# Kernel tuning notes

Measured on AMD Instinct MI355X. Metric: run time of the kernel, lower is better.

The kernel has to match this reference:

```python
import jax, jax.numpy as jnp
import numpy as np

HID, H, KV, D = 2048, 16, 4, 128
B, L = 8, 1024
T = B * L
EPS = 1e-6
NEG = -1e9


def _rms(x, w):
    # RMSNorm over head_dim in fp32
    var = jnp.mean(x.astype(jnp.float32) ** 2, axis=-1, keepdims=True)
    return (x.astype(jnp.float32) * jax.lax.rsqrt(var + EPS)).astype(x.dtype) * w


def _rot_half(x):
    x1, x2 = jnp.split(x, 2, axis=-1)
    return jnp.concatenate([-x2, x1], axis=-1)


def setup_inputs() -> dict:
    key = jax.random.key(0)
    ks = jax.random.split(key, 24)
    inp = {}
    inp['packed_sequence'] = jax.random.normal(ks[0], (T, HID), jnp.float32) * 0.02
    # RoPE tables: positions restart per sample
    pos = jnp.tile(jnp.arange(L, dtype=jnp.float32), B)  # [T]
    inv_freq = 1.0 / (10000.0 ** (jnp.arange(0, D, 2, dtype=jnp.float32) / D))
    ang = pos[:, None] * inv_freq[None, :]  # [T, D/2]
    inp['cos'] = jnp.concatenate([jnp.cos(ang), jnp.cos(ang)], axis=-1)
    inp['sin'] = jnp.concatenate([jnp.sin(ang), jnp.sin(ang)], axis=-1)
    # per-sample causal additive mask [B, L, L]
    causal = jnp.tril(jnp.ones((L, L), bool))
    inp['attn_bias'] = jnp.broadcast_to(jnp.where(causal, 0.0, NEG).astype(jnp.float32), (B, L, L))
    inp['gen_mask'] = jax.random.randint(ks[1], (T,), 0, 2, jnp.int32)
    s = 0.02
    inp['Wq'] = jax.random.normal(ks[2], (H * D, HID), jnp.float32) * s
    inp['bq'] = jnp.zeros((H * D,), jnp.float32)
    inp['Wqg'] = jax.random.normal(ks[3], (H * D, HID), jnp.float32) * s
    inp['bqg'] = jnp.zeros((H * D,), jnp.float32)
    inp['Wk'] = jax.random.normal(ks[4], (KV * D, HID), jnp.float32) * s
    inp['bk'] = jnp.zeros((KV * D,), jnp.float32)
    inp['Wkg'] = jax.random.normal(ks[5], (KV * D, HID), jnp.float32) * s
    inp['bkg'] = jnp.zeros((KV * D,), jnp.float32)
    inp['Wv'] = jax.random.normal(ks[6], (KV * D, HID), jnp.float32) * s
    inp['bv'] = jnp.zeros((KV * D,), jnp.float32)
    inp['Wvg'] = jax.random.normal(ks[7], (KV * D, HID), jnp.float32) * s
    inp['bvg'] = jnp.zeros((KV * D,), jnp.float32)
    inp['Wo'] = jax.random.normal(ks[8], (HID, H * D), jnp.float32) * s
    inp['Wog'] = jax.random.normal(ks[9], (HID, H * D), jnp.float32) * s
    inp['q_norm_w'] = jnp.ones((D,), jnp.float32)
    inp['q_norm_gen_w'] = jnp.ones((D,), jnp.float32)
    inp['k_norm_w'] = jnp.ones((D,), jnp.float32)
    inp['k_norm_gen_w'] = jnp.ones((D,), jnp.float32)
    return inp


def reference(packed_sequence, cos, sin, attn_bias, gen_mask,
              Wq, bq, Wqg, bqg, Wk, bk, Wkg, bkg, Wv, bv, Wvg, bvg,
              Wo, Wog, q_norm_w, q_norm_gen_w, k_norm_w, k_norm_gen_w):
    route = (gen_mask > 0)[:, None]  # [T,1]; und/gen indexes partition tokens -> select
    # dual-path QKV projections (scatter into zero buffers == per-token select)
    q = jnp.where(route, packed_sequence @ Wqg.T + bqg, packed_sequence @ Wq.T + bq)
    k = jnp.where(route, packed_sequence @ Wkg.T + bkg, packed_sequence @ Wk.T + bk)
    v = jnp.where(route, packed_sequence @ Wvg.T + bvg, packed_sequence @ Wv.T + bv)
    q = q.reshape(T, H, D)
    k = k.reshape(T, KV, D)
    v = v.reshape(T, KV, D)
    rh = route[:, :, None]  # [T,1,1]
    # dual-path per-head-dim RMSNorm
    q = jnp.where(rh, _rms(q, q_norm_gen_w), _rms(q, q_norm_w))
    k = jnp.where(rh, _rms(k, k_norm_gen_w), _rms(k, k_norm_w))
    # RoPE (broadcast over heads, unsqueeze_dim=1)
    c, s = cos[:, None, :], sin[:, None, :]
    q = q * c + _rot_half(q) * s
    k = k * c + _rot_half(k) * s
    # GQA: repeat kv heads to H
    k = jnp.repeat(k, H // KV, axis=1)
    v = jnp.repeat(v, H // KV, axis=1)
    # ragged attention, equal sample lens -> batched SDPA with per-sample masks
    qb = q.reshape(B, L, H, D)
    kb = k.reshape(B, L, H, D)
    vb = v.reshape(B, L, H, D)
    scores = jnp.einsum('blhd,bmhd->bhlm', qb, kb) / np.sqrt(D).astype(np.float32)
    scores = scores + attn_bias[:, None, :, :]
    p = jax.nn.softmax(scores, axis=-1)
    o = jnp.einsum('bhlm,bmhd->blhd', p, vb).reshape(T, H * D)
    # dual-path output projection (no bias)
    return jnp.where(route, o @ Wog.T, o @ Wo.T)
```

## Files before the change

kernel.cpp:

```cpp
#include <hip/hip_runtime.h>

#define T_TOK 8192
#define HID   2048
#define NH    16
#define NKV   4
#define HD    128

typedef __attribute__((ext_vector_type(8))) short short8;
typedef __attribute__((ext_vector_type(4))) float f32x4;
typedef __attribute__((ext_vector_type(4))) unsigned short us4;

__device__ __forceinline__ unsigned short f2b(float f) {
  union { float f; unsigned int u; } x; x.f = f;
  unsigned int u = x.u;
  return (unsigned short)((u + 0x7FFFu + ((u >> 16) & 1u)) >> 16);
}
__device__ __forceinline__ float b2f(unsigned short u) {
  union { float f; unsigned int u; } x; x.u = ((unsigned int)u) << 16; return x.f;
}

__device__ __forceinline__ void ld_lds16(const unsigned short* g, unsigned short* l) {
  __builtin_amdgcn_global_load_lds(
      (const __attribute__((address_space(1))) unsigned int*)g,
      (__attribute__((address_space(3))) unsigned int*)l, 16, 0, 0);
}

__device__ __forceinline__ int xcd_swz(int orig, int nwg) {
  int q = nwg >> 3;
  return (orig & 7) * q + (orig >> 3);
}

__device__ __forceinline__ void qkv_map(int orig, int& bx, int& by, int& set) {
  int xcd = orig & 7;
  int wl = orig >> 3;
  int g = wl / 96;
  int rem = wl - g * 96;
  int p = rem >> 1;
  int e = rem & 1;
  bx = (g * 2 + e) * 8 + xcd;
  set = p / 24; by = p - set * 24;
}
__device__ __forceinline__ void out_map(int orig, int& bx, int& by, int& set) {
  int xcd = orig & 7;
  int wl = orig >> 3;
  int g = wl / 64;
  int rem = wl - g * 64;
  int p = rem >> 1;
  int e = rem & 1;
  bx = (g * 2 + e) * 8 + xcd;
  set = p / 16; by = p - set * 16;
}

struct ConvArgs {
  const float* src[9];
  unsigned short* dst[9];
  int blk_end[9];
  const int* gm; int* perm; int* n0p;
};

__global__ __launch_bounds__(256) void convert_all(ConvArgs a) {
  int blk = blockIdx.x;
  int nconv = a.blk_end[8];
  if (blk == nconv) {
    __shared__ int cnt[256];
    int t = threadIdx.x;
    int base = t * 32;
    int c = 0;
#pragma unroll
    for (int i = 0; i < 32; i++) c += (a.gm[base + i] > 0) ? 0 : 1;
    cnt[t] = c;
    __syncthreads();
    for (int off = 1; off < 256; off <<= 1) {
      int add = (t >= off) ? cnt[t - off] : 0;
      __syncthreads();
      cnt[t] += add;
      __syncthreads();
    }
    int incl = cnt[t];
    int total0 = cnt[255];
    int p0 = incl - c;
    int p1 = total0 + base - p0;
#pragma unroll
    for (int i = 0; i < 32; i++) {
      int tok = base + i;
      if (a.gm[tok] > 0) a.perm[p1++] = tok;
      else               a.perm[p0++] = tok;
    }
    if (t == 0) a.n0p[0] = total0;
    return;
  }
  int s = 0;
  while (blk >= a.blk_end[s]) s++;
  int local = blk - (s ? a.blk_end[s - 1] : 0);
  int i = local * 1024 + threadIdx.x * 4;
  float4 v = *(const float4*)(a.src[s] + i);
  us4 o = { f2b(v.x), f2b(v.y), f2b(v.z), f2b(v.w) };
  *(us4*)(a.dst[s] + i) = o;
}

#define BM  128
#define BK  64

__device__ __forceinline__ void gemm_core(
    const unsigned short* __restrict__ Xb,
    const unsigned short* __restrict__ W,
    const float* __restrict__ bias,
    const int* __restrict__ perm,
    int r0, int r1, int col0, int N,
    float* __restrict__ outF, unsigned short* __restrict__ outB,
    unsigned short* As, unsigned short* Bs)
{
  int tid = threadIdx.x;
  int lane = tid & 63, wid = tid >> 6;
  int quad = lane >> 4, l15 = lane & 15;
  int wr = (wid >> 1) * 64, wc = (wid & 1) * 64;
  int lrow = lane >> 3;
  int sc8 = (lane & 7) ^ (lrow & 7);

  const unsigned short* ag[4]; const unsigned short* bg[4];
  unsigned short* al[4]; unsigned short* bl[4];
#pragma unroll
  for (int i = 0; i < 4; i++) {
    int row = wid * 32 + i * 8 + lrow;
    int gr = r0 + row; if (gr > r1 - 1) gr = r1 - 1;
    ag[i] = Xb + (size_t)perm[gr] * HID + sc8 * 8;
    bg[i] = W + (size_t)(col0 + row) * HID + sc8 * 8;
    al[i] = As + (wid * 32 + i * 8) * BK;
    bl[i] = Bs + (wid * 32 + i * 8) * BK;
  }

  f32x4 zero = {0.f, 0.f, 0.f, 0.f};
  f32x4 acc[4][4];
#pragma unroll
  for (int a = 0; a < 4; a++)
#pragma unroll
    for (int b = 0; b < 4; b++) acc[a][b] = zero;

  for (int k0 = 0; k0 < HID; k0 += BK) {
#pragma unroll
    for (int i = 0; i < 4; i++) {
      ld_lds16(ag[i] + k0, al[i]);
      ld_lds16(bg[i] + k0, bl[i]);
    }
    __syncthreads();
#pragma unroll
    for (int kk = 0; kk < 2; kk++) {
      int cswz = ((kk * 4 + quad) ^ (l15 & 7)) * 8;
      short8 af[4], bf[4];
#pragma unroll
      for (int mt = 0; mt < 4; mt++)
        af[mt] = *(const short8*)&As[(wr + mt * 16 + l15) * BK + cswz];
#pragma unroll
      for (int nt = 0; nt < 4; nt++)
        bf[nt] = *(const short8*)&Bs[(wc + nt * 16 + l15) * BK + cswz];
#pragma unroll
      for (int mt = 0; mt < 4; mt++)
#pragma unroll
        for (int nt = 0; nt < 4; nt++)
          acc[mt][nt] = __builtin_amdgcn_mfma_f32_16x16x32_bf16(af[mt], bf[nt], acc[mt][nt], 0, 0, 0);
    }
    __syncthreads();
  }

#pragma unroll
  for (int mt = 0; mt < 4; mt++) {
#pragma unroll
    for (int r = 0; r < 4; r++) {
      int lr = wr + mt * 16 + quad * 4 + r;
      int gr = r0 + lr;
      if (gr >= r1) continue;
      int tok = perm[gr];
#pragma unroll
      for (int nt = 0; nt < 4; nt++) {
        int col = col0 + wc + nt * 16 + l15;
        float v = acc[mt][nt][r];
        if (bias) v += bias[col];
        if (outF) outF[(size_t)tok * N + col] = v;
        else      outB[(size_t)tok * N + col] = f2b(v);
      }
    }
  }
}

#define QKV_GX 64
#define QKV_GY 24
__global__ __launch_bounds__(256, 3) void gemm_qkv(
    const unsigned short* __restrict__ xb,
    const unsigned short* wq0, const unsigned short* wq1,
    const float* bq0, const float* bq1,
    const unsigned short* wk0, const unsigned short* wk1,
    const float* bk0, const float* bk1,
    const unsigned short* wv0, const unsigned short* wv1,
    const float* bv0, const float* bv1,
    unsigned short* qraw, unsigned short* kraw, unsigned short* vb,
    const int* __restrict__ perm, const int* __restrict__ n0p)
{
  __shared__ unsigned short As[BM * BK];
  __shared__ unsigned short Bs[BM * BK];
  int orig = blockIdx.x + QKV_GX * (blockIdx.y + QKV_GY * blockIdx.z);
  int bx, by, set;
  qkv_map(orig, bx, by, set);

  int n0 = n0p[0];
  int r0, r1;
  if (set == 0) { r0 = bx * BM; if (r0 >= n0) return; r1 = (r0 + BM < n0) ? r0 + BM : n0; }
  else          { r0 = n0 + bx * BM; if (r0 >= T_TOK) return; r1 = (r0 + BM < T_TOK) ? r0 + BM : T_TOK; }
  const unsigned short* w; const float* bias;
  unsigned short* ob; int col0, N;
  if (by < 16)      { w = set ? wq1 : wq0; bias = set ? bq1 : bq0; col0 = by * 128;        N = HID; ob = qraw; }
  else if (by < 20) { w = set ? wk1 : wk0; bias = set ? bk1 : bk0; col0 = (by - 16) * 128; N = 512; ob = kraw; }
  else              { w = set ? wv1 : wv0; bias = set ? bv1 : bv0; col0 = (by - 20) * 128; N = 512; ob = vb; }
  gemm_core(xb, w, bias, perm, r0, r1, col0, N, nullptr, ob, As, Bs);
}

#define OUT_GX 64
#define OUT_GY 16
__global__ __launch_bounds__(256, 3) void gemm_out(
    const unsigned short* __restrict__ obuf,
    const unsigned short* wo0, const unsigned short* wo1,
    float* __restrict__ out,
    const int* __restrict__ perm, const int* __restrict__ n0p)
{
  __shared__ unsigned short As[BM * BK];
  __shared__ unsigned short Bs[BM * BK];
  int orig = blockIdx.x + OUT_GX * (blockIdx.y + OUT_GY * blockIdx.z);
  int bx, by, set;
  out_map(orig, bx, by, set);

  int n0 = n0p[0];
  int r0, r1;
  if (set == 0) { r0 = bx * BM; if (r0 >= n0) return; r1 = (r0 + BM < n0) ? r0 + BM : n0; }
  else          { r0 = n0 + bx * BM; if (r0 >= T_TOK) return; r1 = (r0 + BM < T_TOK) ? r0 + BM : T_TOK; }
  gemm_core(obuf, set ? wo1 : wo0, nullptr, perm, r0, r1, by * 128, HID, out, nullptr, As, Bs);
}

#define RR_BLOCKS (T_TOK * (NH + NKV) / 4)

__global__ __launch_bounds__(256) void rope_vtrans(
    const unsigned short* __restrict__ qin, unsigned short* __restrict__ qout,
    const unsigned short* __restrict__ kin, unsigned short* __restrict__ kout,
    const float* __restrict__ cosb, const float* __restrict__ sinb,
    const int* __restrict__ gm,
    const float* __restrict__ qwn, const float* __restrict__ qwg,
    const float* __restrict__ kwn, const float* __restrict__ kwg,
    const unsigned short* __restrict__ vb, unsigned short* __restrict__ vt)
{
  __shared__ unsigned short Vs[64][136];
  if (blockIdx.x >= RR_BLOCKS) {
    int idx = blockIdx.x - RR_BLOCKS;
    int kt = idx & 15, kvh = (idx >> 4) & 3, b = idx >> 6;
    int t = threadIdx.x;
    int kv0 = kt * 64;
    int key = t >> 2, c0 = t & 3;
#pragma unroll
    for (int i = 0; i < 4; i++) {
      int cc = c0 * 4 + i;
      *(short8*)&Vs[key][cc * 8] =
          *(const short8*)(vb + ((size_t)(b * 1024 + kv0 + key) * NKV + kvh) * HD + cc * 8);
    }
    __syncthreads();
    int d = t >> 1, hh = t & 1;
    unsigned short tmp[32];
#pragma unroll
    for (int k = 0; k < 32; k++) tmp[k] = Vs[hh * 32 + k][d];
    size_t base = ((size_t)(b * NKV + kvh) * HD + d) * 1024 + kv0 + hh * 32;
    *(short8*)(vt + base)      = *(short8*)&tmp[0];
    *(short8*)(vt + base + 8)  = *(short8*)&tmp[8];
    *(short8*)(vt + base + 16) = *(short8*)&tmp[16];
    *(short8*)(vt + base + 24) = *(short8*)&tmp[24];
    return;
  }
  int wvid = blockIdx.x * 4 + (threadIdx.x >> 6);
  int lane = threadIdx.x & 63;
  const unsigned short* in; unsigned short* outp;
  const float* wn; const float* wg; int t, h, nh;
  if (wvid < T_TOK * NH) {
    in = qin; outp = qout; wn = qwn; wg = qwg; t = wvid >> 4; h = wvid & 15; nh = NH;
  } else {
    int w2 = wvid - T_TOK * NH;
    in = kin; outp = kout; wn = kwn; wg = kwg; t = w2 >> 2; h = w2 & 3; nh = NKV;
  }
  size_t off = ((size_t)t * nh + h) * HD;
  float x1 = b2f(in[off + lane]), x2 = b2f(in[off + 64 + lane]);
  float ss = x1 * x1 + x2 * x2;
#pragma unroll
  for (int o = 32; o > 0; o >>= 1) ss += __shfl_xor(ss, o, 64);
  float inv = rsqrtf(ss * (1.0f / 128.0f) + 1e-6f);
  const float* w = (gm[t] > 0) ? wg : wn;
  float n1 = x1 * inv * w[lane];
  float n2 = x2 * inv * w[lane + 64];
  float c1 = cosb[t * HD + lane],      s1 = sinb[t * HD + lane];
  float c2 = cosb[t * HD + 64 + lane], s2 = sinb[t * HD + 64 + lane];
  outp[off + lane]      = f2b(n1 * c1 - n2 * s1);
  outp[off + 64 + lane] = f2b(n2 * c2 + n1 * s2);
}

__global__ __launch_bounds__(512, 4) void attn_kernel(
    const unsigned short* __restrict__ qb,
    const unsigned short* __restrict__ kb,
    const unsigned short* __restrict__ vt,
    unsigned short* __restrict__ ob)
{
  __shared__ unsigned short Ks[2][64 * 128];
  __shared__ unsigned short Vt[2][128 * 64];
  __shared__ unsigned short Ps[8 * 16 * 64];
  int orig = blockIdx.x + 16 * (blockIdx.y + 4 * blockIdx.z);
  int wg = xcd_swz(orig, 16 * 4 * 8);
  int pslot = wg % 16, kvh = (wg / 16) % 4, b = wg / 64;

  int tid = threadIdx.x, lane = tid & 63, wid = tid >> 6;
  int quad = lane >> 4, l15 = lane & 15;
  int h = kvh * 4 + (wid >> 1);
  int g = wid & 1;
  const float sc = 0.088388347648318447f;
  f32x4 zero = {0.f, 0.f, 0.f, 0.f};

  int skey = (wid << 2) + (lane >> 4);
  int kswz = ((lane & 15) ^ (skey & 7)) * 8;
  int sd   = (wid << 3) + (lane >> 3);
  int vswz = ((lane & 7) ^ (sd & 7)) * 8;

  auto stageKV = [&](int buf, int kv0) {
#pragma unroll
    for (int i = 0; i < 2; i++) {
      int key = i * 32 + skey;
      ld_lds16(kb + ((size_t)(b * 1024 + kv0 + key) * NKV + kvh) * HD + kswz,
               &Ks[buf][(size_t)(i * 32 + (wid << 2)) * 128]);
    }
#pragma unroll
    for (int i = 0; i < 2; i++) {
      int d = i * 64 + sd;
      ld_lds16(vt + ((size_t)(b * NKV + kvh) * HD + d) * 1024 + kv0 + vswz,
               &Vt[buf][(size_t)(i * 64 + (wid << 3)) * 64]);
    }
  };

  for (int half = 0; half < 2; half++) {
    int a = half ? (31 - pslot) : pslot;
    int q0 = a * 32;
    int qrow = q0 + g * 16 + l15;
    size_t qoff = ((size_t)(b * 1024 + qrow) * NH + h) * HD;
    short8 qfr[4];
#pragma unroll
    for (int kk = 0; kk < 4; kk++)
      qfr[kk] = *(const short8*)(qb + qoff + kk * 32 + quad * 8);

    f32x4 oacc[8];
#pragma unroll
    for (int i = 0; i < 8; i++) oacc[i] = zero;
    float lpart[4] = {0.f, 0.f, 0.f, 0.f};

    int ktiles = a / 2 + 1;
    stageKV(0, 0);
    int cur = 0;

    for (int kt = 0; kt < ktiles; kt++) {
      int kv0 = kt * 64;
      bool hasnext = (kt + 1 < ktiles);
      if (hasnext) {
        stageKV(cur ^ 1, kv0 + 64);
        asm volatile("s_waitcnt vmcnt(4)" ::: "memory");
      } else {
        asm volatile("s_waitcnt vmcnt(0)" ::: "memory");
      }
      __builtin_amdgcn_s_barrier();
      __builtin_amdgcn_sched_barrier(0);
      const unsigned short* ksb = Ks[cur];
      const unsigned short* vvb = Vt[cur];
      bool lastt = (kt == ktiles - 1);

      f32x4 s[4];
      __builtin_amdgcn_s_setprio(1);
#pragma unroll
      for (int g4 = 0; g4 < 4; g4++) {
        f32x4 acc = zero;
#pragma unroll
        for (int kk = 0; kk < 4; kk++) {
          short8 bfr = *(const short8*)&ksb[(g4 * 16 + l15) * 128 + ((kk * 4 + quad) ^ (l15 & 7)) * 8];
          acc = __builtin_amdgcn_mfma_f32_16x16x32_bf16(qfr[kk], bfr, acc, 0, 0, 0);
        }
        s[g4] = acc;
      }
      __builtin_amdgcn_s_setprio(0);

      int rowb = q0 + g * 16 + quad * 4;
#pragma unroll
      for (int g4 = 0; g4 < 4; g4++) {
        int col = kv0 + g4 * 16 + l15;
        int k8 = g4 * 2 + (l15 >> 3);
#pragma unroll
        for (int r = 0; r < 4; r++) {
          float p = __expf(s[g4][r] * sc);
          if (lastt && col > rowb + r) p = 0.f;
          lpart[r] += p;
          int row = quad * 4 + r;
          Ps[wid * 1024 + row * 64 + ((k8 ^ (row & 7)) * 8 + (l15 & 7))] = f2b(p);
        }
      }

      __builtin_amdgcn_s_setprio(1);
#pragma unroll
      for (int kk = 0; kk < 2; kk++) {
        short8 pa = *(const short8*)&Ps[wid * 1024 + l15 * 64 + ((kk * 4 + quad) ^ (l15 & 7)) * 8];
#pragma unroll
        for (int dg = 0; dg < 8; dg++) {
          short8 vf = *(const short8*)&vvb[(dg * 16 + l15) * 64 + ((kk * 4 + quad) ^ (l15 & 7)) * 8];
          oacc[dg] = __builtin_amdgcn_mfma_f32_16x16x32_bf16(pa, vf, oacc[dg], 0, 0, 0);
        }
      }
      __builtin_amdgcn_s_setprio(0);

      __builtin_amdgcn_s_barrier();
      __builtin_amdgcn_sched_barrier(0);
      cur ^= 1;
    }

#pragma unroll
    for (int r = 0; r < 4; r++) {
      float v = lpart[r];
#pragma unroll
      for (int o = 8; o > 0; o >>= 1) v += __shfl_xor(v, o, 64);
      lpart[r] = 1.0f / v;
    }
#pragma unroll
    for (int dg = 0; dg < 8; dg++)
#pragma unroll
      for (int r = 0; r < 4; r++) {
        int row = q0 + g * 16 + quad * 4 + r;
        ob[((size_t)(b * 1024 + row) * NH + h) * HD + dg * 16 + l15] =
            f2b(oacc[dg][r] * lpart[r]);
      }
  }
}

extern "C" void kernel_launch(void* const* d_in, const int* in_sizes, int n_in,
                              void* d_out, int out_size, void* d_ws, size_t ws_size,
                              hipStream_t stream) {
  const float* x    = (const float*)d_in[0];
  const float* cosb = (const float*)d_in[1];
  const float* sinb = (const float*)d_in[2];
  const int*   gm   = (const int*)d_in[4];
  const float* Wq   = (const float*)d_in[5];
  const float* bq   = (const float*)d_in[6];
  const float* Wqg  = (const float*)d_in[7];
  const float* bqg  = (const float*)d_in[8];
  const float* Wk   = (const float*)d_in[9];
  const float* bk   = (const float*)d_in[10];
  const float* Wkg  = (const float*)d_in[11];
  const float* bkg  = (const float*)d_in[12];
  const float* Wv   = (const float*)d_in[13];
  const float* bv   = (const float*)d_in[14];
  const float* Wvg  = (const float*)d_in[15];
  const float* bvg  = (const float*)d_in[16];
  const float* Wo   = (const float*)d_in[17];
  const float* Wog  = (const float*)d_in[18];
  const float* qnw  = (const float*)d_in[19];
  const float* qngw = (const float*)d_in[20];
  const float* knw  = (const float*)d_in[21];
  const float* kngw = (const float*)d_in[22];
  float* out = (float*)d_out;

  char* wsb = (char*)d_ws;
  size_t off = 0;
  auto alloc = [&](size_t bytes) -> char* {
    char* p = wsb + off;
    off += (bytes + 255) & ~(size_t)255;
    return p;
  };
  int* perm = (int*)alloc((size_t)T_TOK * 4);
  int* n0p  = (int*)alloc(4);
  unsigned short* xb  = (unsigned short*)alloc((size_t)T_TOK * HID * 2);
  unsigned short* wq0 = (unsigned short*)alloc((size_t)HID * HID * 2);
  unsigned short* wq1 = (unsigned short*)alloc((size_t)HID * HID * 2);
  unsigned short* wk0 = (unsigned short*)alloc((size_t)512 * HID * 2);
  unsigned short* wk1 = (unsigned short*)alloc((size_t)512 * HID * 2);
  unsigned short* wv0 = (unsigned short*)alloc((size_t)512 * HID * 2);
  unsigned short* wv1 = (unsigned short*)alloc((size_t)512 * HID * 2);
  unsigned short* wo0 = (unsigned short*)alloc((size_t)HID * HID * 2);
  unsigned short* wo1 = (unsigned short*)alloc((size_t)HID * HID * 2);
  unsigned short* qraw = (unsigned short*)alloc((size_t)T_TOK * HID * 2);
  unsigned short* kraw = (unsigned short*)alloc((size_t)T_TOK * 512 * 2);
  unsigned short* vbuf = (unsigned short*)alloc((size_t)T_TOK * 512 * 2);
  unsigned short* vtb  = (unsigned short*)alloc((size_t)T_TOK * 512 * 2);
  unsigned short* qbuf = (unsigned short*)alloc((size_t)T_TOK * HID * 2);
  unsigned short* kbuf = (unsigned short*)alloc((size_t)T_TOK * 512 * 2);
  unsigned short* obuf = qraw;

  ConvArgs ca;
  const float* srcs[9] = {x, Wq, Wqg, Wk, Wkg, Wv, Wvg, Wo, Wog};
  unsigned short* dsts[9] = {xb, wq0, wq1, wk0, wk1, wv0, wv1, wo0, wo1};
  int ns[9] = {T_TOK * HID, HID * HID, HID * HID, 512 * HID, 512 * HID,
               512 * HID, 512 * HID, HID * HID, HID * HID};
  int cum = 0;
  for (int i = 0; i < 9; i++) {
    ca.src[i] = srcs[i]; ca.dst[i] = dsts[i];
    cum += ns[i] / 1024; ca.blk_end[i] = cum;
  }
  ca.gm = gm; ca.perm = perm; ca.n0p = n0p;
  convert_all<<<dim3(cum + 1), dim3(256), 0, stream>>>(ca);

  gemm_qkv<<<dim3(QKV_GX, QKV_GY, 2), dim3(256), 0, stream>>>(
      xb, wq0, wq1, bq, bqg, wk0, wk1, bk, bkg, wv0, wv1, bv, bvg,
      qraw, kraw, vbuf, perm, n0p);

  rope_vtrans<<<dim3(RR_BLOCKS + 512), dim3(256), 0, stream>>>(
      qraw, qbuf, kraw, kbuf, cosb, sinb, gm, qnw, qngw, knw, kngw, vbuf, vtb);

  attn_kernel<<<dim3(16, 4, 8), dim3(512), 0, stream>>>(qbuf, kbuf, vtb, obuf);

  gemm_out<<<dim3(OUT_GX, OUT_GY, 2), dim3(256), 0, stream>>>(obuf, wo0, wo1, out, perm, n0p);
}
```

Measured before the change: 555.9 us.

## Fuse RMSNorm, RoPE and softmax scale into the QKV GEMM epilogue

The QKV GEMM epilogue now applies the bias, the per-head RMSNorm (a cross-wave sum of squares through shared memory) and RoPE through a staged LDS tile, and writes normalized q/k directly. Q also gets the 1/sqrt(D) scale there, so the attention kernel drops its multiply. This removes the separate rope pass and its round trip of raw q/k through global memory, leaving only a small V-transpose kernel. The cost is a larger GEMM epilogue with extra barriers and LDS, which may reduce occupancy, plus a separate obuf allocation.

Measured after the change: 529.7 us. -4.7%, faster.

```diff
diff --git a/kernel.cpp b/kernel.cpp
--- a/kernel.cpp
+++ b/kernel.cpp
@@ -100,6 +100,7 @@
 
 #define BM  128
 #define BK  64
+#define TSTR 136
 
 __device__ __forceinline__ void gemm_core(
     const unsigned short* __restrict__ Xb,
@@ -108,7 +109,11 @@
     const int* __restrict__ perm,
     int r0, int r1, int col0, int N,
     float* __restrict__ outF, unsigned short* __restrict__ outB,
-    unsigned short* As, unsigned short* Bs)
+    unsigned short* As, unsigned short* Bs,
+    unsigned short* tile, float* ssb,
+    const float* __restrict__ wnorm,
+    const float* __restrict__ cosbp, const float* __restrict__ sinbp,
+    float oscale)
 {
   int tid = threadIdx.x;
   int lane = tid & 63, wid = tid >> 6;
@@ -162,22 +167,104 @@
     __syncthreads();
   }
 
-#pragma unroll
-  for (int mt = 0; mt < 4; mt++) {
+  if (wnorm == nullptr) {
+#pragma unroll
+    for (int mt = 0; mt < 4; mt++) {
+#pragma unroll
+      for (int r = 0; r < 4; r++) {
+        int lr = wr + mt * 16 + quad * 4 + r;
+        int gr = r0 + lr;
+        if (gr >= r1) continue;
+        int tok = perm[gr];
+#pragma unroll
+        for (int nt = 0; nt < 4; nt++) {
+          int col = col0 + wc + nt * 16 + l15;
+          float v = acc[mt][nt][r];
+          if (bias) v += bias[col];
+          if (outF) outF[(size_t)tok * N + col] = v;
+          else      outB[(size_t)tok * N + col] = f2b(v);
+        }
+      }
+    }
+    return;
+  }
+
+  float ssl[4][4];
+#pragma unroll
+  for (int mt = 0; mt < 4; mt++)
+#pragma unroll
+    for (int r = 0; r < 4; r++) ssl[mt][r] = 0.f;
+#pragma unroll
+  for (int nt = 0; nt < 4; nt++) {
+    float bcol = bias[col0 + wc + nt * 16 + l15];
+#pragma unroll
+    for (int mt = 0; mt < 4; mt++)
+#pragma unroll
+      for (int r = 0; r < 4; r++) {
+        float v = acc[mt][nt][r] + bcol;
+        acc[mt][nt][r] = v;
+        ssl[mt][r] += v * v;
+      }
+  }
+#pragma unroll
+  for (int mt = 0; mt < 4; mt++)
+#pragma unroll
+    for (int r = 0; r < 4; r++) {
+      float s = ssl[mt][r];
+      s += __shfl_xor(s, 1, 64); s += __shfl_xor(s, 2, 64);
+      s += __shfl_xor(s, 4, 64); s += __shfl_xor(s, 8, 64);
+      ssl[mt][r] = s;
+    }
+  if (l15 == 0) {
+#pragma unroll
+    for (int mt = 0; mt < 4; mt++)
+#pragma unroll
+      for (int r = 0; r < 4; r++)
+        ssb[(wid & 1) * 128 + wr + mt * 16 + quad * 4 + r] = ssl[mt][r];
+  }
+  __syncthreads();
+
+  float wv_[4];
+#pragma unroll
+  for (int nt = 0; nt < 4; nt++) wv_[nt] = wnorm[wc + nt * 16 + l15];
+#pragma unroll
+  for (int mt = 0; mt < 4; mt++)
 #pragma unroll
     for (int r = 0; r < 4; r++) {
       int lr = wr + mt * 16 + quad * 4 + r;
-      int gr = r0 + lr;
-      if (gr >= r1) continue;
-      int tok = perm[gr];
-#pragma unroll
-      for (int nt = 0; nt < 4; nt++) {
-        int col = col0 + wc + nt * 16 + l15;
-        float v = acc[mt][nt][r];
-        if (bias) v += bias[col];
-        if (outF) outF[(size_t)tok * N + col] = v;
-        else      outB[(size_t)tok * N + col] = f2b(v);
-      }
+      float inv = rsqrtf((ssb[lr] + ssb[128 + lr]) * (1.0f / 128.0f) + 1e-6f);
+#pragma unroll
+      for (int nt = 0; nt < 4; nt++)
+        tile[lr * TSTR + wc + nt * 16 + l15] = f2b(acc[mt][nt][r] * inv * wv_[nt]);
+    }
+  __syncthreads();
+
+  int row = tid >> 1, hf = tid & 1;
+  int gr = r0 + row;
+  if (gr < r1) {
+    int tok = perm[gr];
+    const short8* ta = (const short8*)&tile[row * TSTR + hf * 64];
+    const short8* tb = (const short8*)&tile[row * TSTR + (hf ^ 1) * 64];
+    const float* cb = cosbp + (size_t)tok * HD + hf * 64;
+    const float* sb = sinbp + (size_t)tok * HD + hf * 64;
+#pragma unroll
+    for (int j = 0; j < 8; j++) {
+      short8 xa = ta[j], xb = tb[j];
+      float4 c1 = *(const float4*)(cb + j * 8);
+      float4 c2 = *(const float4*)(cb + j * 8 + 4);
+      float4 s1 = *(const float4*)(sb + j * 8);
+      float4 s2 = *(const float4*)(sb + j * 8 + 4);
+      float cc[8] = {c1.x, c1.y, c1.z, c1.w, c2.x, c2.y, c2.z, c2.w};
+      float sn[8] = {s1.x, s1.y, s1.z, s1.w, s2.x, s2.y, s2.z, s2.w};
+      short8 o;
+#pragma unroll
+      for (int e = 0; e < 8; e++) {
+        float xv = b2f((unsigned short)xa[e]);
+        float pv = b2f((unsigned short)xb[e]);
+        float ov = hf == 0 ? (xv * cc[e] - pv * sn[e]) : (xv * cc[e] + pv * sn[e]);
+        o[e] = (short)f2b(ov * oscale);
+      }
+      *(short8*)&outB[(size_t)tok * N + col0 + hf * 64 + j * 8] = o;
     }
   }
 }
@@ -192,11 +279,16 @@
     const float* bk0, const float* bk1,
     const unsigned short* wv0, const unsigned short* wv1,
     const float* bv0, const float* bv1,
-    unsigned short* qraw, unsigned short* kraw, unsigned short* vb,
+    unsigned short* qbuf, unsigned short* kbuf, unsigned short* vb,
+    const float* qnw, const float* qngw, const float* knw, const float* kngw,
+    const float* cosb, const float* sinb,
     const int* __restrict__ perm, const int* __restrict__ n0p)
 {
-  __shared__ unsigned short As[BM * BK];
-  __shared__ unsigned short Bs[BM * BK];
+  __shared__ __align__(16) unsigned short smem[128 * TSTR];
+  __shared__ float ssb[2 * 128];
+  unsigned short* As = smem;
+  unsigned short* Bs = smem + 8192;
+
   int orig = blockIdx.x + QKV_GX * (blockIdx.y + QKV_GY * blockIdx.z);
   int bx, by, set;
   qkv_map(orig, bx, by, set);
@@ -205,12 +297,21 @@
   int r0, r1;
   if (set == 0) { r0 = bx * BM; if (r0 >= n0) return; r1 = (r0 + BM < n0) ? r0 + BM : n0; }
   else          { r0 = n0 + bx * BM; if (r0 >= T_TOK) return; r1 = (r0 + BM < T_TOK) ? r0 + BM : T_TOK; }
-  const unsigned short* w; const float* bias;
-  unsigned short* ob; int col0, N;
-  if (by < 16)      { w = set ? wq1 : wq0; bias = set ? bq1 : bq0; col0 = by * 128;        N = HID; ob = qraw; }
-  else if (by < 20) { w = set ? wk1 : wk0; bias = set ? bk1 : bk0; col0 = (by - 16) * 128; N = 512; ob = kraw; }
-  else              { w = set ? wv1 : wv0; bias = set ? bv1 : bv0; col0 = (by - 20) * 128; N = 512; ob = vb; }
-  gemm_core(xb, w, bias, perm, r0, r1, col0, N, nullptr, ob, As, Bs);
+
+  const unsigned short* w; const float* bias; const float* wn;
+  unsigned short* ob; int col0, N; float osc;
+  if (by < 16) {
+    w = set ? wq1 : wq0; bias = set ? bq1 : bq0; col0 = by * 128; N = HID; ob = qbuf;
+    wn = set ? qngw : qnw; osc = 0.088388347648318447f;
+  } else if (by < 20) {
+    w = set ? wk1 : wk0; bias = set ? bk1 : bk0; col0 = (by - 16) * 128; N = 512; ob = kbuf;
+    wn = set ? kngw : knw; osc = 1.0f;
+  } else {
+    w = set ? wv1 : wv0; bias = set ? bv1 : bv0; col0 = (by - 20) * 128; N = 512; ob = vb;
+    wn = nullptr; osc = 1.0f;
+  }
+  gemm_core(xb, w, bias, perm, r0, r1, col0, N, nullptr, ob, As, Bs,
+            smem, ssb, wn, cosb, sinb, osc);
 }
 
 #define OUT_GX 64
@@ -221,8 +322,8 @@
     float* __restrict__ out,
     const int* __restrict__ perm, const int* __restrict__ n0p)
 {
-  __shared__ unsigned short As[BM * BK];
-  __shared__ unsigned short Bs[BM * BK];
+  __shared__ __align__(16) unsigned short As[BM * BK];
+  __shared__ __align__(16) unsigned short Bs[BM * BK];
   int orig = blockIdx.x + OUT_GX * (blockIdx.y + OUT_GY * blockIdx.z);
   int bx, by, set;
   out_map(orig, bx, by, set);
@@ -231,68 +332,33 @@
   int r0, r1;
   if (set == 0) { r0 = bx * BM; if (r0 >= n0) return; r1 = (r0 + BM < n0) ? r0 + BM : n0; }
   else          { r0 = n0 + bx * BM; if (r0 >= T_TOK) return; r1 = (r0 + BM < T_TOK) ? r0 + BM : T_TOK; }
-  gemm_core(obuf, set ? wo1 : wo0, nullptr, perm, r0, r1, by * 128, HID, out, nullptr, As, Bs);
-}
-
-#define RR_BLOCKS (T_TOK * (NH + NKV) / 4)
-
-__global__ __launch_bounds__(256) void rope_vtrans(
-    const unsigned short* __restrict__ qin, unsigned short* __restrict__ qout,
-    const unsigned short* __restrict__ kin, unsigned short* __restrict__ kout,
-    const float* __restrict__ cosb, const float* __restrict__ sinb,
-    const int* __restrict__ gm,
-    const float* __restrict__ qwn, const float* __restrict__ qwg,
-    const float* __restrict__ kwn, const float* __restrict__ kwg,
-    const unsigned short* __restrict__ vb, unsigned short* __restrict__ vt)
-{
+  gemm_core(obuf, set ? wo1 : wo0, nullptr, perm, r0, r1, by * 128, HID, out, nullptr,
+            As, Bs, nullptr, nullptr, nullptr, nullptr, nullptr, 1.0f);
+}
+
+__global__ __launch_bounds__(256) void vtrans(const unsigned short* __restrict__ vb,
+                                              unsigned short* __restrict__ vt) {
   __shared__ unsigned short Vs[64][136];
-  if (blockIdx.x >= RR_BLOCKS) {
-    int idx = blockIdx.x - RR_BLOCKS;
-    int kt = idx & 15, kvh = (idx >> 4) & 3, b = idx >> 6;
-    int t = threadIdx.x;
-    int kv0 = kt * 64;
-    int key = t >> 2, c0 = t & 3;
-#pragma unroll
-    for (int i = 0; i < 4; i++) {
-      int cc = c0 * 4 + i;
-      *(short8*)&Vs[key][cc * 8] =
-          *(const short8*)(vb + ((size_t)(b * 1024 + kv0 + key) * NKV + kvh) * HD + cc * 8);
-    }
-    __syncthreads();
-    int d = t >> 1, hh = t & 1;
-    unsigned short tmp[32];
-#pragma unroll
-    for (int k = 0; k < 32; k++) tmp[k] = Vs[hh * 32 + k][d];
-    size_t base = ((size_t)(b * NKV + kvh) * HD + d) * 1024 + kv0 + hh * 32;
-    *(short8*)(vt + base)      = *(short8*)&tmp[0];
-    *(short8*)(vt + base + 8)  = *(short8*)&tmp[8];
-    *(short8*)(vt + base + 16) = *(short8*)&tmp[16];
-    *(short8*)(vt + base + 24) = *(short8*)&tmp[24];
-    return;
-  }
-  int wvid = blockIdx.x * 4 + (threadIdx.x >> 6);
-  int lane = threadIdx.x & 63;
-  const unsigned short* in; unsigned short* outp;
-  const float* wn; const float* wg; int t, h, nh;
-  if (wvid < T_TOK * NH) {
-    in = qin; outp = qout; wn = qwn; wg = qwg; t = wvid >> 4; h = wvid & 15; nh = NH;
-  } else {
-    int w2 = wvid - T_TOK * NH;
-    in = kin; outp = kout; wn = kwn; wg = kwg; t = w2 >> 2; h = w2 & 3; nh = NKV;
-  }
-  size_t off = ((size_t)t * nh + h) * HD;
-  float x1 = b2f(in[off + lane]), x2 = b2f(in[off + 64 + lane]);
-  float ss = x1 * x1 + x2 * x2;
-#pragma unroll
-  for (int o = 32; o > 0; o >>= 1) ss += __shfl_xor(ss, o, 64);
-  float inv = rsqrtf(ss * (1.0f / 128.0f) + 1e-6f);
-  const float* w = (gm[t] > 0) ? wg : wn;
-  float n1 = x1 * inv * w[lane];
-  float n2 = x2 * inv * w[lane + 64];
-  float c1 = cosb[t * HD + lane],      s1 = sinb[t * HD + lane];
-  float c2 = cosb[t * HD + 64 + lane], s2 = sinb[t * HD + 64 + lane];
-  outp[off + lane]      = f2b(n1 * c1 - n2 * s1);
-  outp[off + 64 + lane] = f2b(n2 * c2 + n1 * s2);
+  int kt = blockIdx.x, kvh = blockIdx.y, b = blockIdx.z;
+  int t = threadIdx.x;
+  int kv0 = kt * 64;
+  int key = t >> 2, c0 = t & 3;
+#pragma unroll
+  for (int i = 0; i < 4; i++) {
+    int cc = c0 * 4 + i;
+    *(short8*)&Vs[key][cc * 8] =
+        *(const short8*)(vb + ((size_t)(b * 1024 + kv0 + key) * NKV + kvh) * HD + cc * 8);
+  }
+  __syncthreads();
+  int d = t >> 1, hh = t & 1;
+  unsigned short tmp[32];
+#pragma unroll
+  for (int k = 0; k < 32; k++) tmp[k] = Vs[hh * 32 + k][d];
+  size_t base = ((size_t)(b * NKV + kvh) * HD + d) * 1024 + kv0 + hh * 32;
+  *(short8*)(vt + base)      = *(short8*)&tmp[0];
+  *(short8*)(vt + base + 8)  = *(short8*)&tmp[8];
+  *(short8*)(vt + base + 16) = *(short8*)&tmp[16];
+  *(short8*)(vt + base + 24) = *(short8*)&tmp[24];
 }
 
 __global__ __launch_bounds__(512, 4) void attn_kernel(
@@ -312,7 +378,6 @@
   int quad = lane >> 4, l15 = lane & 15;
   int h = kvh * 4 + (wid >> 1);
   int g = wid & 1;
-  const float sc = 0.088388347648318447f;
   f32x4 zero = {0.f, 0.f, 0.f, 0.f};
 
   int skey = (wid << 2) + (lane >> 4);
@@ -390,7 +455,7 @@
         int k8 = g4 * 2 + (l15 >> 3);
 #pragma unroll
         for (int r = 0; r < 4; r++) {
-          float p = __expf(s[g4][r] * sc);
+          float p = __expf(s[g4][r]);
           if (lastt && col > rowb + r) p = 0.f;
           lpart[r] += p;
           int row = quad * 4 + r;
@@ -478,13 +543,11 @@
   unsigned short* wv1 = (unsigned short*)alloc((size_t)512 * HID * 2);
   unsigned short* wo0 = (unsigned short*)alloc((size_t)HID * HID * 2);
   unsigned short* wo1 = (unsigned short*)alloc((size_t)HID * HID * 2);
-  unsigned short* qraw = (unsigned short*)alloc((size_t)T_TOK * HID * 2);
-  unsigned short* kraw = (unsigned short*)alloc((size_t)T_TOK * 512 * 2);
   unsigned short* vbuf = (unsigned short*)alloc((size_t)T_TOK * 512 * 2);
   unsigned short* vtb  = (unsigned short*)alloc((size_t)T_TOK * 512 * 2);
   unsigned short* qbuf = (unsigned short*)alloc((size_t)T_TOK * HID * 2);
   unsigned short* kbuf = (unsigned short*)alloc((size_t)T_TOK * 512 * 2);
-  unsigned short* obuf = qraw;
+  unsigned short* obuf = (unsigned short*)alloc((size_t)T_TOK * HID * 2);
 
   ConvArgs ca;
   const float* srcs[9] = {x, Wq, Wqg, Wk, Wkg, Wv, Wvg, Wo, Wog};
@@ -501,10 +564,9 @@
 
   gemm_qkv<<<dim3(QKV_GX, QKV_GY, 2), dim3(256), 0, stream>>>(
       xb, wq0, wq1, bq, bqg, wk0, wk1, bk, bkg, wv0, wv1, bv, bvg,
-      qraw, kraw, vbuf, perm, n0p);
-
-  rope_vtrans<<<dim3(RR_BLOCKS + 512), dim3(256), 0, stream>>>(
-      qraw, qbuf, kraw, kbuf, cosb, sinb, gm, qnw, qngw, knw, kngw, vbuf, vtb);
+      qbuf, kbuf, vbuf, qnw, qngw, knw, kngw, cosb, sinb, perm, n0p);
+
+  vtrans<<<dim3(16, 4, 8), dim3(256), 0, stream>>>(vbuf, vtb);
 
   attn_kernel<<<dim3(16, 4, 8), dim3(512), 0, stream>>>(qbuf, kbuf, vtb, obuf);
 
```
